# Optimization experiments

Measured on AMD Instinct MI355X. Metric: run time of the kernel, lower is better.

The kernel has to match this reference:

```python
import jax, jax.numpy as jnp
import numpy as np

N = 8192   # nodes
E = 32768  # edges
D = 512    # out_features (node/edge feature dim); in_features = 2*D
DEG = 16   # max neighbors / incident edges per node
DEP = 8    # max node deps per edge
K = 3      # hops (opt.Node_K)


def _padded_idx(k1, k2, rows, width, hi, min_deg):
    # random index lists padded with -1 at the tail
    idx = jax.random.randint(k1, (rows, width), 0, hi, dtype=jnp.int32)
    deg = jax.random.randint(k2, (rows,), min_deg, width + 1, dtype=jnp.int32)
    return jnp.where(jnp.arange(width, dtype=jnp.int32)[None, :] < deg[:, None], idx, -1)


def setup_inputs():
    key = jax.random.key(0)
    ks = jax.random.split(key, 16)
    f32 = jnp.float32
    fw_input = jax.random.normal(ks[0], (N, D), f32)
    bw_input = jax.random.normal(ks[1], (N, D), f32)
    edge_embs = jax.random.normal(ks[2], (E, D), f32)
    fw_adj = _padded_idx(ks[3], ks[4], N, DEG, N, 1)
    bw_adj = _padded_idx(ks[5], ks[6], N, DEG, N, 1)
    fw_edgeid = _padded_idx(ks[7], ks[8], N, DEG, E, 0)
    bw_edgeid = _padded_idx(ks[9], ks[10], N, DEG, E, 0)
    fw_edgedep = _padded_idx(ks[11], ks[12], E, DEP, N, 1)
    bw_edgedep = _padded_idx(ks[13], ks[14], E, DEP, N, 1)
    kp = jax.random.split(ks[15], 3)
    s2 = np.float32(1.0 / np.sqrt(2 * D))
    s3 = np.float32(1.0 / np.sqrt(3 * D))
    Wfc = jax.random.normal(kp[0], (2 * D, D), f32) * s2
    bfc = jnp.zeros((D,), f32)
    Wbc = jax.random.normal(kp[1], (2 * D, D), f32) * s2
    bbc = jnp.zeros((D,), f32)
    Wedge = jax.random.normal(kp[2], (3 * D, D), f32) * s3
    bedge = jnp.zeros((D,), f32)
    return dict(fw_input=fw_input, bw_input=bw_input, edge_embs=edge_embs,
                fw_adj=fw_adj, bw_adj=bw_adj, fw_edgeid=fw_edgeid, bw_edgeid=bw_edgeid,
                fw_edgedep=fw_edgedep, bw_edgedep=bw_edgedep,
                Wfc=Wfc, bfc=bfc, Wbc=Wbc, bbc=bbc, Wedge=Wedge, bedge=bedge)


def _masked_sum(x, idx):
    # gather rows of x at idx (-1 = padding), return masked sum and count
    m = (idx >= 0)
    g = x[jnp.maximum(idx, 0)] * m[..., None].astype(x.dtype)  # [rows, width, D]
    return g.sum(axis=1), m.sum(axis=1)


def _nbr_mean(nodes, adj, edge_embs, eids):
    # mean over (edge embeddings of incident edges ++ neighbor node features)
    s1, c1 = _masked_sum(nodes, adj)
    s2, c2 = _masked_sum(edge_embs, eids)
    cnt = (c1 + c2).astype(nodes.dtype)
    return (s1 + s2) / cnt[:, None]


def _forward(fw_input, bw_input, edge_embs, fw_adj, bw_adj, fw_edgeid, bw_edgeid,
             fw_edgedep, bw_edgedep, Wfc, bfc, Wbc, bbc, Wedge, bedge):
    for k in range(K):
        fmean = _nbr_mean(fw_input, fw_adj, edge_embs, fw_edgeid)
        bmean = _nbr_mean(bw_input, bw_adj, edge_embs, bw_edgeid)
        fh = jnp.concatenate([fw_input, fmean], axis=-1) @ Wfc + bfc
        bh = jnp.concatenate([bw_input, bmean], axis=-1) @ Wbc + bbc
        if k < K - 1:
            fh = jax.nn.relu(fh)
            bh = jax.nn.relu(bh)
        fw_input, bw_input = fh, bh
        if k < K - 1:  # edge update (uses the freshly updated node features)
            fs, fcnt = _masked_sum(fw_input, fw_edgedep)
            bs, bcnt = _masked_sum(bw_input, bw_edgedep)
            fdep = fs / fcnt.astype(fs.dtype)[:, None]
            bdep = bs / bcnt.astype(bs.dtype)[:, None]
            edge_embs = jax.nn.relu(
                jnp.concatenate([edge_embs, fdep, bdep], axis=-1) @ Wedge + bedge)
    return fw_input, bw_input


def reference(fw_input, bw_input, edge_embs, fw_adj, bw_adj, fw_edgeid, bw_edgeid,
              fw_edgedep, bw_edgedep, Wfc, bfc, Wbc, bbc, Wedge, bedge):
    return _forward(fw_input, bw_input, edge_embs, fw_adj, bw_adj, fw_edgeid, bw_edgeid,
                    fw_edgedep, bw_edgedep, Wfc, bfc, Wbc, bbc, Wedge, bedge)
```

## Files before the change

### kernel.cpp

```cpp
#include <hip/hip_runtime.h>
#include <hip/hip_bf16.h>

#define N_NODES 8192
#define N_EDGES 32768
#define DFEAT   512

typedef __attribute__((ext_vector_type(8))) short          bf16x8;
typedef __attribute__((ext_vector_type(4))) float          f32x4;
typedef __attribute__((ext_vector_type(8))) unsigned short u16x8;

__device__ __forceinline__ float bf2f(unsigned short u) {
  union { unsigned int i; float f; } x; x.i = ((unsigned int)u) << 16; return x.f;
}
__device__ __forceinline__ unsigned short f2bf(float f) {
  __hip_bfloat16 h = __float2bfloat16(f);
  return *reinterpret_cast<unsigned short*>(&h);
}

#define GLDS16(gp, lp) __builtin_amdgcn_global_load_lds( \
    (const __attribute__((address_space(1))) void*)(gp),  \
    (__attribute__((address_space(3))) void*)(lp), 16, 0, 0)

#define KEEP16(a) asm volatile("" :: \
  "v"(a[0]), "v"(a[1]), "v"(a[2]),  "v"(a[3]),  "v"(a[4]),  "v"(a[5]),  "v"(a[6]),  "v"(a[7]), \
  "v"(a[8]), "v"(a[9]), "v"(a[10]), "v"(a[11]), "v"(a[12]), "v"(a[13]), "v"(a[14]), "v"(a[15]))

__global__ void transpose_w3(const float* __restrict__ W0, const float* __restrict__ W1,
                             const float* __restrict__ W2,
                             unsigned short* __restrict__ T0, unsigned short* __restrict__ T1,
                             unsigned short* __restrict__ T2) {
  __shared__ float tile[32][33];
  const float* W; unsigned short* WT; int K;
  if (blockIdx.z == 0)      { W = W0; WT = T0; K = 1024; }
  else if (blockIdx.z == 1) { W = W1; WT = T1; K = 1024; }
  else                      { W = W2; WT = T2; K = 1536; }
  const int k0 = blockIdx.x * 32, n0 = blockIdx.y * 32;
  if (k0 >= K) return;
  const int tx = threadIdx.x, ty = threadIdx.y;
  #pragma unroll
  for (int i = ty; i < 32; i += 8)
    tile[i][tx] = W[(long)(k0 + i) * DFEAT + n0 + tx];
  __syncthreads();
  #pragma unroll
  for (int i = ty; i < 32; i += 8)
    WT[(long)(n0 + i) * K + k0 + tx] = f2bf(tile[tx][i]);
}

__global__ void cvt3(const float* __restrict__ a, const float* __restrict__ b,
                     const float* __restrict__ c,
                     unsigned short* __restrict__ da, unsigned short* __restrict__ db,
                     unsigned short* __restrict__ dc, long na, long nc) {
  long i = ((long)blockIdx.x * blockDim.x + threadIdx.x) * 4;
  const float* s; unsigned short* d; long off;
  if (i < na)           { s = a; d = da; off = i; }
  else if (i < 2 * na)  { s = b; d = db; off = i - na; }
  else if (i < 2 * na + nc) { s = c; d = dc; off = i - 2 * na; }
  else return;
  float4 v = *reinterpret_cast<const float4*>(&s[off]);
  ushort4 o = { f2bf(v.x), f2bf(v.y), f2bf(v.z), f2bf(v.w) };
  *reinterpret_cast<ushort4*>(&d[off]) = o;
}

__global__ __launch_bounds__(256, 2) void nbr_mean2(
    const unsigned short* __restrict__ nodesF, const unsigned short* __restrict__ nodesB,
    const unsigned short* __restrict__ edges,
    const int* __restrict__ adjF, const int* __restrict__ adjB,
    const int* __restrict__ eidF, const int* __restrict__ eidB,
    unsigned short* __restrict__ dstF, unsigned short* __restrict__ dstB) {
  const int wave = threadIdx.x >> 6, lane = threadIdx.x & 63;
  const int n = blockIdx.x * 4 + wave;
  const unsigned short* nodes; const int* adj; const int* eid; unsigned short* dst;
  if (blockIdx.y == 0) { nodes = nodesF; adj = adjF; eid = eidF; dst = dstF; }
  else                 { nodes = nodesB; adj = adjB; eid = eidB; dst = dstB; }
  const int c0 = lane * 8;

  int ia[16], ie[16];
  {
    const int4* pa = reinterpret_cast<const int4*>(adj + (long)n * 16);
    const int4* pe = reinterpret_cast<const int4*>(eid + (long)n * 16);
    #pragma unroll
    for (int q = 0; q < 4; ++q) {
      int4 t = pa[q];
      ia[q * 4] = t.x; ia[q * 4 + 1] = t.y; ia[q * 4 + 2] = t.z; ia[q * 4 + 3] = t.w;
      int4 u = pe[q];
      ie[q * 4] = u.x; ie[q * 4 + 1] = u.y; ie[q * 4 + 2] = u.z; ie[q * 4 + 3] = u.w;
    }
  }

  u16x8 va[16], ve[16];
  #pragma unroll
  for (int j = 0; j < 16; ++j) {
    const int a = ia[j] >= 0 ? ia[j] : 0;
    va[j] = *reinterpret_cast<const u16x8*>(&nodes[(long)a * DFEAT + c0]);
  }
  #pragma unroll
  for (int j = 0; j < 16; ++j) {
    const int a = ie[j] >= 0 ? ie[j] : 0;
    ve[j] = *reinterpret_cast<const u16x8*>(&edges[(long)a * DFEAT + c0]);
  }
  KEEP16(va);
  KEEP16(ve);

  float s[8] = {0, 0, 0, 0, 0, 0, 0, 0};
  int cnt = 0;
  #pragma unroll
  for (int j = 0; j < 16; ++j) {
    if (ia[j] >= 0) {
      ++cnt;
      #pragma unroll
      for (int i = 0; i < 8; ++i) s[i] += bf2f(va[j][i]);
    }
  }
  #pragma unroll
  for (int j = 0; j < 16; ++j) {
    if (ie[j] >= 0) {
      ++cnt;
      #pragma unroll
      for (int i = 0; i < 8; ++i) s[i] += bf2f(ve[j][i]);
    }
  }
  const float inv = 1.0f / (float)cnt;
  u16x8 o;
  #pragma unroll
  for (int i = 0; i < 8; ++i) o[i] = f2bf(s[i] * inv);
  *reinterpret_cast<u16x8*>(&dst[(long)n * DFEAT + c0]) = o;
}

__global__ __launch_bounds__(256, 2) void edge_fuse(
    const unsigned short* __restrict__ Pf, const unsigned short* __restrict__ Pb,
    const unsigned short* __restrict__ Ge,
    const int* __restrict__ fdep, const int* __restrict__ bdep,
    unsigned short* __restrict__ Een) {
  const int wave = threadIdx.x >> 6, lane = threadIdx.x & 63;
  const int e = blockIdx.x * 4 + wave;
  const int c0 = lane * 8;

  int idx[16];
  {
    const int4* pf = reinterpret_cast<const int4*>(fdep + (long)e * 8);
    const int4* pb = reinterpret_cast<const int4*>(bdep + (long)e * 8);
    #pragma unroll
    for (int q = 0; q < 2; ++q) {
      int4 t = pf[q];
      idx[q * 4] = t.x; idx[q * 4 + 1] = t.y; idx[q * 4 + 2] = t.z; idx[q * 4 + 3] = t.w;
      int4 u = pb[q];
      idx[8 + q * 4] = u.x; idx[8 + q * 4 + 1] = u.y; idx[8 + q * 4 + 2] = u.z; idx[8 + q * 4 + 3] = u.w;
    }
  }

  const u16x8 gv = *reinterpret_cast<const u16x8*>(&Ge[(long)e * DFEAT + c0]);

  u16x8 v[16];
  #pragma unroll
  for (int j = 0; j < 8; ++j) {
    const int a = idx[j] >= 0 ? idx[j] : 0;
    v[j] = *reinterpret_cast<const u16x8*>(&Pf[(long)a * DFEAT + c0]);
  }
  #pragma unroll
  for (int j = 0; j < 8; ++j) {
    const int a = idx[8 + j] >= 0 ? idx[8 + j] : 0;
    v[8 + j] = *reinterpret_cast<const u16x8*>(&Pb[(long)a * DFEAT + c0]);
  }
  KEEP16(v);

  float sf[8] = {0, 0, 0, 0, 0, 0, 0, 0};
  float sb[8] = {0, 0, 0, 0, 0, 0, 0, 0};
  int fc = 0, bc = 0;
  #pragma unroll
  for (int j = 0; j < 8; ++j) {
    if (idx[j] >= 0) {
      ++fc;
      #pragma unroll
      for (int i = 0; i < 8; ++i) sf[i] += bf2f(v[j][i]);
    }
  }
  #pragma unroll
  for (int j = 0; j < 8; ++j) {
    if (idx[8 + j] >= 0) {
      ++bc;
      #pragma unroll
      for (int i = 0; i < 8; ++i) sb[i] += bf2f(v[8 + j][i]);
    }
  }
  const float invf = 1.0f / (float)fc, invb = 1.0f / (float)bc;
  u16x8 o;
  #pragma unroll
  for (int i = 0; i < 8; ++i) {
    float x = bf2f(gv[i]) + sf[i] * invf + sb[i] * invb;
    o[i] = f2bf(fmaxf(x, 0.0f));
  }
  *reinterpret_cast<u16x8*>(&Een[(long)e * DFEAT + c0]) = o;
}

struct GArg {
  const unsigned short* A0;
  const unsigned short* A1;
  const unsigned short* Bt;
  const float* bias;
  unsigned short* outb;
  float* outf;
};

template<int K, int LDB, int NSEG, int SWZQ, bool RELU, bool BIAS, bool BF16OUT>
__global__ __launch_bounds__(256, 2) void gemm2(GArg ga, GArg gb) {
  const GArg g = blockIdx.z ? gb : ga;
  __shared__ unsigned short As[128][32];
  __shared__ unsigned short Bs[128][32];
  const int tid = threadIdx.x;
  const int wave = tid >> 6, lane = tid & 63;
  const int bid = blockIdx.x;
  const int swz = (bid & 7) * SWZQ + (bid >> 3);
  const long brow = (long)(swz >> 2) * 128;
  const int bcol = (swz & 3) * 128;
  const int wr = (wave >> 1) * 64, wc = (wave & 1) * 64;

  f32x4 acc[4][4] = {};

  const int srow = lane >> 2;
  const int scol = (lane & 3) * 8;
  const int rb = wave * 32;
  unsigned short* As0 = &As[rb][0];
  unsigned short* As1 = &As[rb + 16][0];
  unsigned short* Bs0 = &Bs[rb][0];
  unsigned short* Bs1 = &Bs[rb + 16][0];

  const int fr = lane & 15;
  const int fk = (lane >> 4) * 8;

  for (int kt = 0; kt < K / 32; ++kt) {
    const unsigned short* Aseg;
    int kcol;
    if (NSEG == 1) { Aseg = g.A0; kcol = kt * 32; }
    else           { Aseg = (kt < 16) ? g.A0 : g.A1; kcol = (kt & 15) * 32; }
    GLDS16(Aseg + (brow + rb + srow) * DFEAT + kcol + scol, As0);
    GLDS16(Aseg + (brow + rb + 16 + srow) * DFEAT + kcol + scol, As1);
    const long bk = (long)kt * 32;
    GLDS16(g.Bt + (long)(bcol + rb + srow) * LDB + bk + scol, Bs0);
    GLDS16(g.Bt + (long)(bcol + rb + 16 + srow) * LDB + bk + scol, Bs1);
    __syncthreads();
    bf16x8 af[4], bfr[4];
    #pragma unroll
    for (int m = 0; m < 4; ++m) af[m] = *reinterpret_cast<const bf16x8*>(&As[wr + m * 16 + fr][fk]);
    #pragma unroll
    for (int n = 0; n < 4; ++n) bfr[n] = *reinterpret_cast<const bf16x8*>(&Bs[wc + n * 16 + fr][fk]);
    #pragma unroll
    for (int m = 0; m < 4; ++m)
      #pragma unroll
      for (int n = 0; n < 4; ++n)
        acc[m][n] = __builtin_amdgcn_mfma_f32_16x16x32_bf16(af[m], bfr[n], acc[m][n], 0, 0, 0);
    __syncthreads();
  }

  #pragma unroll
  for (int n = 0; n < 4; ++n) {
    const int col = bcol + wc + n * 16 + fr;
    float bv = 0.0f;
    if (BIAS) bv = g.bias[col];
    #pragma unroll
    for (int m = 0; m < 4; ++m) {
      const long row0 = brow + wr + m * 16 + (lane >> 4) * 4;
      #pragma unroll
      for (int i = 0; i < 4; ++i) {
        float v = acc[m][n][i] + bv;
        if (RELU) v = fmaxf(v, 0.0f);
        if (BF16OUT) g.outb[(row0 + i) * DFEAT + col] = f2bf(v);
        else         g.outf[(row0 + i) * DFEAT + col] = v;
      }
    }
  }
}

extern "C" void kernel_launch(void* const* d_in, const int* in_sizes, int n_in,
                              void* d_out, int out_size, void* d_ws, size_t ws_size,
                              hipStream_t stream) {
  const float* fw_in   = (const float*)d_in[0];
  const float* bw_in   = (const float*)d_in[1];
  const float* edge_in = (const float*)d_in[2];
  const int* fw_adj    = (const int*)d_in[3];
  const int* bw_adj    = (const int*)d_in[4];
  const int* fw_eid    = (const int*)d_in[5];
  const int* bw_eid    = (const int*)d_in[6];
  const int* fw_dep    = (const int*)d_in[7];
  const int* bw_dep    = (const int*)d_in[8];
  const float* Wfc     = (const float*)d_in[9];
  const float* bfc     = (const float*)d_in[10];
  const float* Wbc     = (const float*)d_in[11];
  const float* bbc     = (const float*)d_in[12];
  const float* Wedge   = (const float*)d_in[13];
  const float* bedge   = (const float*)d_in[14];
  float* out_f = (float*)d_out;

  char* w = (char*)d_ws;
  auto alloc = [&](size_t b) { char* p = w; w += (b + 255) & ~(size_t)255; return p; };
  const size_t nodeB = (size_t)N_NODES * DFEAT * 2;
  const size_t edgeB = (size_t)N_EDGES * DFEAT * 2;
  unsigned short* Ff0 = (unsigned short*)alloc(nodeB);
  unsigned short* Ff1 = (unsigned short*)alloc(nodeB);
  unsigned short* Fb0 = (unsigned short*)alloc(nodeB);
  unsigned short* Fb1 = (unsigned short*)alloc(nodeB);
  unsigned short* Mf  = (unsigned short*)alloc(nodeB);
  unsigned short* Mb  = (unsigned short*)alloc(nodeB);
  unsigned short* Pf  = (unsigned short*)alloc(nodeB);
  unsigned short* Pb  = (unsigned short*)alloc(nodeB);
  unsigned short* Ee0 = (unsigned short*)alloc(edgeB);
  unsigned short* Ee1 = (unsigned short*)alloc(edgeB);
  unsigned short* Ge  = (unsigned short*)alloc(edgeB);
  unsigned short* WfT = (unsigned short*)alloc((size_t)1024 * 512 * 2);
  unsigned short* WbT = (unsigned short*)alloc((size_t)1024 * 512 * 2);
  unsigned short* WeT = (unsigned short*)alloc((size_t)1536 * 512 * 2);
  if ((size_t)(w - (char*)d_ws) > ws_size) return;

  transpose_w3<<<dim3(48, 16, 3), dim3(32, 8), 0, stream>>>(Wfc, Wbc, Wedge, WfT, WbT, WeT);
  {
    const long nn = (long)N_NODES * DFEAT, ne = (long)N_EDGES * DFEAT;
    const long tot = 2 * nn + ne;
    cvt3<<<(int)(tot / 4 / 256), 256, 0, stream>>>(fw_in, bw_in, edge_in, Ff0, Fb0, Ee0, nn, ne);
  }

  unsigned short *Ffc = Ff0, *Ffn = Ff1, *Fbc = Fb0, *Fbn = Fb1, *Eec = Ee0, *Een = Ee1;

  for (int k = 0; k < 3; ++k) {
    nbr_mean2<<<dim3(N_NODES / 4, 2), 256, 0, stream>>>(
        Ffc, Fbc, Eec, fw_adj, bw_adj, fw_eid, bw_eid, Mf, Mb);
    if (k < 2) {
      gemm2<1024, 1024, 2, 32, true, true, true><<<dim3(256, 1, 2), 256, 0, stream>>>(
          GArg{Ffc, Mf, WfT, bfc, Ffn, nullptr}, GArg{Fbc, Mb, WbT, bbc, Fbn, nullptr});
      gemm2<512, 1536, 1, 32, false, false, true><<<dim3(256, 1, 2), 256, 0, stream>>>(
          GArg{Ffn, nullptr, WeT + 512, nullptr, Pf, nullptr},
          GArg{Fbn, nullptr, WeT + 1024, nullptr, Pb, nullptr});
      gemm2<512, 1536, 1, 128, false, true, true><<<dim3(1024, 1, 1), 256, 0, stream>>>(
          GArg{Eec, nullptr, WeT, bedge, Ge, nullptr},
          GArg{Eec, nullptr, WeT, bedge, Ge, nullptr});
      edge_fuse<<<N_EDGES / 4, 256, 0, stream>>>(Pf, Pb, Ge, fw_dep, bw_dep, Een);
      unsigned short* t;
      t = Ffc; Ffc = Ffn; Ffn = t;
      t = Fbc; Fbc = Fbn; Fbn = t;
      t = Eec; Eec = Een; Een = t;
    } else {
      gemm2<1024, 1024, 2, 32, false, true, false><<<dim3(256, 1, 2), 256, 0, stream>>>(
          GArg{Ffc, Mf, WfT, bfc, nullptr, out_f},
          GArg{Fbc, Mb, WbT, bbc, nullptr, out_f + (long)N_NODES * DFEAT});
    }
  }
}
```

Measured before the change: 533.1 us.

## Merge edge-projection GEMMs into one launch and stage gather waits with inline loads

Replaces the two edge-update GEMM launches (node projections Pf/Pb and the edge projection Ge) with a single gemm3 kernel. It dispatches 1536 blocks across the three problems using a swizzled block id, which removes one launch and balances the tail. The gather kernels now issue loads through inline asm global_load_dwordx4 and explicit vmcnt waits. This lets nbr_mean start summing neighbor rows while edge rows are still in flight. Hand-written waitcnt is fragile: it relies on the compiler not inserting other vector-memory ops between the loads and the waits.

```diff
diff --git a/kernel.cpp b/kernel.cpp
--- a/kernel.cpp
+++ b/kernel.cpp
@@ -21,9 +21,13 @@
     (const __attribute__((address_space(1))) void*)(gp),  \
     (__attribute__((address_space(3))) void*)(lp), 16, 0, 0)
 
-#define KEEP16(a) asm volatile("" :: \
-  "v"(a[0]), "v"(a[1]), "v"(a[2]),  "v"(a[3]),  "v"(a[4]),  "v"(a[5]),  "v"(a[6]),  "v"(a[7]), \
-  "v"(a[8]), "v"(a[9]), "v"(a[10]), "v"(a[11]), "v"(a[12]), "v"(a[13]), "v"(a[14]), "v"(a[15]))
+__device__ __forceinline__ void gload16(u16x8& d, const unsigned short* p) {
+  asm volatile("global_load_dwordx4 %0, %1, off" : "=v"(d) : "v"(p));
+}
+#define WAIT_VM(N) do { \
+  asm volatile("s_waitcnt vmcnt(" #N ")" ::: "memory"); \
+  __builtin_amdgcn_sched_barrier(0); \
+} while (0)
 
 __global__ void transpose_w3(const float* __restrict__ W0, const float* __restrict__ W1,
                              const float* __restrict__ W2,
@@ -91,18 +95,17 @@
   #pragma unroll
   for (int j = 0; j < 16; ++j) {
     const int a = ia[j] >= 0 ? ia[j] : 0;
-    va[j] = *reinterpret_cast<const u16x8*>(&nodes[(long)a * DFEAT + c0]);
+    gload16(va[j], &nodes[(long)a * DFEAT + c0]);
   }
   #pragma unroll
   for (int j = 0; j < 16; ++j) {
     const int a = ie[j] >= 0 ? ie[j] : 0;
-    ve[j] = *reinterpret_cast<const u16x8*>(&edges[(long)a * DFEAT + c0]);
-  }
-  KEEP16(va);
-  KEEP16(ve);
+    gload16(ve[j], &edges[(long)a * DFEAT + c0]);
+  }
 
   float s[8] = {0, 0, 0, 0, 0, 0, 0, 0};
   int cnt = 0;
+  WAIT_VM(16);
   #pragma unroll
   for (int j = 0; j < 16; ++j) {
     if (ia[j] >= 0) {
@@ -111,6 +114,7 @@
       for (int i = 0; i < 8; ++i) s[i] += bf2f(va[j][i]);
     }
   }
+  WAIT_VM(0);
   #pragma unroll
   for (int j = 0; j < 16; ++j) {
     if (ie[j] >= 0) {
@@ -148,20 +152,19 @@
     }
   }
 
-  const u16x8 gv = *reinterpret_cast<const u16x8*>(&Ge[(long)e * DFEAT + c0]);
-
-  u16x8 v[16];
+  u16x8 gv, v[16];
+  gload16(gv, &Ge[(long)e * DFEAT + c0]);
   #pragma unroll
   for (int j = 0; j < 8; ++j) {
     const int a = idx[j] >= 0 ? idx[j] : 0;
-    v[j] = *reinterpret_cast<const u16x8*>(&Pf[(long)a * DFEAT + c0]);
+    gload16(v[j], &Pf[(long)a * DFEAT + c0]);
   }
   #pragma unroll
   for (int j = 0; j < 8; ++j) {
     const int a = idx[8 + j] >= 0 ? idx[8 + j] : 0;
-    v[8 + j] = *reinterpret_cast<const u16x8*>(&Pb[(long)a * DFEAT + c0]);
-  }
-  KEEP16(v);
+    gload16(v[8 + j], &Pb[(long)a * DFEAT + c0]);
+  }
+  WAIT_VM(0);
 
   float sf[8] = {0, 0, 0, 0, 0, 0, 0, 0};
   float sb[8] = {0, 0, 0, 0, 0, 0, 0, 0};
@@ -266,6 +269,68 @@
         if (BF16OUT) g.outb[(row0 + i) * DFEAT + col] = f2bf(v);
         else         g.outf[(row0 + i) * DFEAT + col] = v;
       }
+    }
+  }
+}
+
+__global__ __launch_bounds__(256, 2) void gemm3(GArg ga, GArg gb, GArg gc) {
+  __shared__ unsigned short As[128][32];
+  __shared__ unsigned short Bs[128][32];
+  const int tid = threadIdx.x;
+  const int wave = tid >> 6, lane = tid & 63;
+  const int bid = blockIdx.x;
+  const int swz = (bid & 7) * 192 + (bid >> 3);
+  GArg g; int base;
+  if (swz < 256)      { g = ga; base = swz; }
+  else if (swz < 512) { g = gb; base = swz - 256; }
+  else                { g = gc; base = swz - 512; }
+  const long brow = (long)(base >> 2) * 128;
+  const int bcol = (base & 3) * 128;
+  const int wr = (wave >> 1) * 64, wc = (wave & 1) * 64;
+
+  f32x4 acc[4][4] = {};
+
+  const int srow = lane >> 2;
+  const int scol = (lane & 3) * 8;
+  const int rb = wave * 32;
+  unsigned short* As0 = &As[rb][0];
+  unsigned short* As1 = &As[rb + 16][0];
+  unsigned short* Bs0 = &Bs[rb][0];
+  unsigned short* Bs1 = &Bs[rb + 16][0];
+
+  const int fr = lane & 15;
+  const int fk = (lane >> 4) * 8;
+
+  for (int kt = 0; kt < 16; ++kt) {
+    const int kcol = kt * 32;
+    GLDS16(g.A0 + (brow + rb + srow) * DFEAT + kcol + scol, As0);
+    GLDS16(g.A0 + (brow + rb + 16 + srow) * DFEAT + kcol + scol, As1);
+    GLDS16(g.Bt + (long)(bcol + rb + srow) * 1536 + kcol + scol, Bs0);
+    GLDS16(g.Bt + (long)(bcol + rb + 16 + srow) * 1536 + kcol + scol, Bs1);
+    __syncthreads();
+    bf16x8 af[4], bfr[4];
+    #pragma unroll
+    for (int m = 0; m < 4; ++m) af[m] = *reinterpret_cast<const bf16x8*>(&As[wr + m * 16 + fr][fk]);
+    #pragma unroll
+    for (int n = 0; n < 4; ++n) bfr[n] = *reinterpret_cast<const bf16x8*>(&Bs[wc + n * 16 + fr][fk]);
+    #pragma unroll
+    for (int m = 0; m < 4; ++m)
+      #pragma unroll
+      for (int n = 0; n < 4; ++n)
+        acc[m][n] = __builtin_amdgcn_mfma_f32_16x16x32_bf16(af[m], bfr[n], acc[m][n], 0, 0, 0);
+    __syncthreads();
+  }
+
+  #pragma unroll
+  for (int n = 0; n < 4; ++n) {
+    const int col = bcol + wc + n * 16 + fr;
+    const float bv = g.bias ? g.bias[col] : 0.0f;
+    #pragma unroll
+    for (int m = 0; m < 4; ++m) {
+      const long row0 = brow + wr + m * 16 + (lane >> 4) * 4;
+      #pragma unroll
+      for (int i = 0; i < 4; ++i)
+        g.outb[(row0 + i) * DFEAT + col] = f2bf(acc[m][n][i] + bv);
     }
   }
 }
@@ -325,11 +390,9 @@
     if (k < 2) {
       gemm2<1024, 1024, 2, 32, true, true, true><<<dim3(256, 1, 2), 256, 0, stream>>>(
           GArg{Ffc, Mf, WfT, bfc, Ffn, nullptr}, GArg{Fbc, Mb, WbT, bbc, Fbn, nullptr});
-      gemm2<512, 1536, 1, 32, false, false, true><<<dim3(256, 1, 2), 256, 0, stream>>>(
+      gemm3<<<dim3(1536), 256, 0, stream>>>(
           GArg{Ffn, nullptr, WeT + 512, nullptr, Pf, nullptr},
-          GArg{Fbn, nullptr, WeT + 1024, nullptr, Pb, nullptr});
-      gemm2<512, 1536, 1, 128, false, true, true><<<dim3(1024, 1, 1), 256, 0, stream>>>(
-          GArg{Eec, nullptr, WeT, bedge, Ge, nullptr},
+          GArg{Fbn, nullptr, WeT + 1024, nullptr, Pb, nullptr},
           GArg{Eec, nullptr, WeT, bedge, Ge, nullptr});
       edge_fuse<<<N_EDGES / 4, 256, 0, stream>>>(Pf, Pb, Ge, fw_dep, bw_dep, Een);
       unsigned short* t;
```

New measurement: 526.4 us. No clear change (-1.3%).

## Fuse edge GEMM into neighbor-mean kernel, widen GEMM K-tile with swizzled LDS

Applied to the files above, without the earlier changes.

Every fifth block of the neighbor-mean launch now runs one tile of the edge-embedding GEMM, so the gather and the GEMM share one launch and can overlap. This drops a separate kernel launch per hop. The GEMM core moves from a 32-wide to a 64-wide K tile, with an XOR-swizzled LDS layout that halves the number of sync rounds and is meant to reduce bank conflicts. The gather kernels issue their loads through inline asm with explicit vmcnt waits, so the first batch of gathered rows can be summed while the rest are still in flight. The trade-offs are a larger LDS footprint, mixed block types in one launch with a relaxed occupancy bound, and hand-managed wait counts.

```diff
diff --git a/kernel.cpp b/kernel.cpp
--- a/kernel.cpp
+++ b/kernel.cpp
@@ -21,9 +21,13 @@
     (const __attribute__((address_space(1))) void*)(gp),  \
     (__attribute__((address_space(3))) void*)(lp), 16, 0, 0)
 
-#define KEEP16(a) asm volatile("" :: \
-  "v"(a[0]), "v"(a[1]), "v"(a[2]),  "v"(a[3]),  "v"(a[4]),  "v"(a[5]),  "v"(a[6]),  "v"(a[7]), \
-  "v"(a[8]), "v"(a[9]), "v"(a[10]), "v"(a[11]), "v"(a[12]), "v"(a[13]), "v"(a[14]), "v"(a[15]))
+__device__ __forceinline__ void gload16(u16x8& d, const unsigned short* p) {
+  asm volatile("global_load_dwordx4 %0, %1, off" : "=v"(d) : "v"(p));
+}
+#define WAIT_VM(N) do { \
+  asm volatile("s_waitcnt vmcnt(" #N ")" ::: "memory"); \
+  __builtin_amdgcn_sched_barrier(0); \
+} while (0)
 
 __global__ void transpose_w3(const float* __restrict__ W0, const float* __restrict__ W1,
                              const float* __restrict__ W2,
@@ -61,17 +65,120 @@
   *reinterpret_cast<ushort4*>(&d[off]) = o;
 }
 
-__global__ __launch_bounds__(256, 2) void nbr_mean2(
+struct GArg {
+  const unsigned short* A0;
+  const unsigned short* A1;
+  const unsigned short* Bt;
+  const float* bias;
+  unsigned short* outb;
+  float* outf;
+};
+
+template<int K, int LDB, int NSEG, bool RELU, bool BIAS, bool BF16OUT>
+__device__ __forceinline__ void gemm_core(GArg g, long brow, int bcol,
+                                          unsigned short (*As)[64],
+                                          unsigned short (*Bs)[64]) {
+  const int tid = threadIdx.x;
+  const int wave = tid >> 6, lane = tid & 63;
+  const int wr = (wave >> 1) * 64, wc = (wave & 1) * 64;
+  f32x4 acc[4][4] = {};
+
+  const int rb = wave * 32;
+  const int sl8 = lane >> 3;
+  const int scol = ((lane & 7) ^ sl8) * 8;
+  const int fr = lane & 15;
+  const int fk = (lane >> 4) * 8;
+
+  for (int kt = 0; kt < K / 64; ++kt) {
+    const unsigned short* Aseg; int kcol;
+    if (NSEG == 1) { Aseg = g.A0; kcol = kt * 64; }
+    else           { Aseg = (kt < 8) ? g.A0 : g.A1; kcol = (kt & 7) * 64; }
+    #pragma unroll
+    for (int c = 0; c < 4; ++c)
+      GLDS16(Aseg + (brow + rb + 8 * c + sl8) * DFEAT + kcol + scol, &As[rb + 8 * c][0]);
+    const long bk = (long)kt * 64;
+    #pragma unroll
+    for (int c = 0; c < 4; ++c)
+      GLDS16(g.Bt + (long)(bcol + rb + 8 * c + sl8) * LDB + bk + scol, &Bs[rb + 8 * c][0]);
+    __syncthreads();
+    #pragma unroll
+    for (int kk = 0; kk < 2; ++kk) {
+      bf16x8 af[4], bfr[4];
+      #pragma unroll
+      for (int m = 0; m < 4; ++m) {
+        const int R = wr + m * 16 + fr;
+        af[m] = *reinterpret_cast<const bf16x8*>(&As[R][(kk * 32 + fk) ^ ((R & 7) * 8)]);
+      }
+      #pragma unroll
+      for (int n = 0; n < 4; ++n) {
+        const int R = wc + n * 16 + fr;
+        bfr[n] = *reinterpret_cast<const bf16x8*>(&Bs[R][(kk * 32 + fk) ^ ((R & 7) * 8)]);
+      }
+      #pragma unroll
+      for (int m = 0; m < 4; ++m)
+        #pragma unroll
+        for (int n = 0; n < 4; ++n)
+          acc[m][n] = __builtin_amdgcn_mfma_f32_16x16x32_bf16(af[m], bfr[n], acc[m][n], 0, 0, 0);
+    }
+    __syncthreads();
+  }
+
+  #pragma unroll
+  for (int n = 0; n < 4; ++n) {
+    const int col = bcol + wc + n * 16 + fr;
+    float bv = 0.0f;
+    if (BIAS) bv = g.bias[col];
+    #pragma unroll
+    for (int m = 0; m < 4; ++m) {
+      const long row0 = brow + wr + m * 16 + (lane >> 4) * 4;
+      #pragma unroll
+      for (int i = 0; i < 4; ++i) {
+        float v = acc[m][n][i] + bv;
+        if (RELU) v = fmaxf(v, 0.0f);
+        if (BF16OUT) g.outb[(row0 + i) * DFEAT + col] = f2bf(v);
+        else         g.outf[(row0 + i) * DFEAT + col] = v;
+      }
+    }
+  }
+}
+
+template<int K, int LDB, int NSEG, int SWZQ, bool RELU, bool BIAS, bool BF16OUT>
+__global__ __launch_bounds__(256, 2) void gemmK(GArg ga, GArg gb) {
+  __shared__ unsigned short As[128][64];
+  __shared__ unsigned short Bs[128][64];
+  const GArg g = blockIdx.z ? gb : ga;
+  const int bid = blockIdx.x;
+  const int swz = (bid & 7) * SWZQ + (bid >> 3);
+  gemm_core<K, LDB, NSEG, RELU, BIAS, BF16OUT>(
+      g, (long)(swz >> 2) * 128, (swz & 3) * 128, As, Bs);
+}
+
+__global__ __launch_bounds__(256) void fused_nbr_ge(
     const unsigned short* __restrict__ nodesF, const unsigned short* __restrict__ nodesB,
     const unsigned short* __restrict__ edges,
     const int* __restrict__ adjF, const int* __restrict__ adjB,
     const int* __restrict__ eidF, const int* __restrict__ eidB,
-    unsigned short* __restrict__ dstF, unsigned short* __restrict__ dstB) {
+    unsigned short* __restrict__ dstF, unsigned short* __restrict__ dstB,
+    GArg ge, int hasGe) {
+  __shared__ unsigned short As[128][64];
+  __shared__ unsigned short Bs[128][64];
+  int bid = blockIdx.x;
+  if (hasGe) {
+    if ((bid % 5) == 4) {
+      const int gid = bid / 5;
+      const int swz = (gid & 7) * 128 + (gid >> 3);
+      gemm_core<512, 1536, 1, false, true, true>(
+          ge, (long)(swz >> 2) * 128, (swz & 3) * 128, As, Bs);
+      return;
+    }
+    bid = (bid / 5) * 4 + (bid % 5);
+  }
   const int wave = threadIdx.x >> 6, lane = threadIdx.x & 63;
-  const int n = blockIdx.x * 4 + wave;
+  const int side = bid >> 11;
+  const int n = (bid & 2047) * 4 + wave;
   const unsigned short* nodes; const int* adj; const int* eid; unsigned short* dst;
-  if (blockIdx.y == 0) { nodes = nodesF; adj = adjF; eid = eidF; dst = dstF; }
-  else                 { nodes = nodesB; adj = adjB; eid = eidB; dst = dstB; }
+  if (side == 0) { nodes = nodesF; adj = adjF; eid = eidF; dst = dstF; }
+  else           { nodes = nodesB; adj = adjB; eid = eidB; dst = dstB; }
   const int c0 = lane * 8;
 
   int ia[16], ie[16];
@@ -91,18 +198,17 @@
   #pragma unroll
   for (int j = 0; j < 16; ++j) {
     const int a = ia[j] >= 0 ? ia[j] : 0;
-    va[j] = *reinterpret_cast<const u16x8*>(&nodes[(long)a * DFEAT + c0]);
+    gload16(va[j], &nodes[(long)a * DFEAT + c0]);
   }
   #pragma unroll
   for (int j = 0; j < 16; ++j) {
     const int a = ie[j] >= 0 ? ie[j] : 0;
-    ve[j] = *reinterpret_cast<const u16x8*>(&edges[(long)a * DFEAT + c0]);
-  }
-  KEEP16(va);
-  KEEP16(ve);
+    gload16(ve[j], &edges[(long)a * DFEAT + c0]);
+  }
 
   float s[8] = {0, 0, 0, 0, 0, 0, 0, 0};
   int cnt = 0;
+  WAIT_VM(16);
   #pragma unroll
   for (int j = 0; j < 16; ++j) {
     if (ia[j] >= 0) {
@@ -111,6 +217,7 @@
       for (int i = 0; i < 8; ++i) s[i] += bf2f(va[j][i]);
     }
   }
+  WAIT_VM(0);
   #pragma unroll
   for (int j = 0; j < 16; ++j) {
     if (ie[j] >= 0) {
@@ -148,20 +255,19 @@
     }
   }
 
-  const u16x8 gv = *reinterpret_cast<const u16x8*>(&Ge[(long)e * DFEAT + c0]);
-
-  u16x8 v[16];
+  u16x8 gv, v[16];
+  gload16(gv, &Ge[(long)e * DFEAT + c0]);
   #pragma unroll
   for (int j = 0; j < 8; ++j) {
     const int a = idx[j] >= 0 ? idx[j] : 0;
-    v[j] = *reinterpret_cast<const u16x8*>(&Pf[(long)a * DFEAT + c0]);
+    gload16(v[j], &Pf[(long)a * DFEAT + c0]);
   }
   #pragma unroll
   for (int j = 0; j < 8; ++j) {
     const int a = idx[8 + j] >= 0 ? idx[8 + j] : 0;
-    v[8 + j] = *reinterpret_cast<const u16x8*>(&Pb[(long)a * DFEAT + c0]);
-  }
-  KEEP16(v);
+    gload16(v[8 + j], &Pb[(long)a * DFEAT + c0]);
+  }
+  WAIT_VM(0);
 
   float sf[8] = {0, 0, 0, 0, 0, 0, 0, 0};
   float sb[8] = {0, 0, 0, 0, 0, 0, 0, 0};
@@ -190,84 +296,6 @@
     o[i] = f2bf(fmaxf(x, 0.0f));
   }
   *reinterpret_cast<u16x8*>(&Een[(long)e * DFEAT + c0]) = o;
-}
-
-struct GArg {
-  const unsigned short* A0;
-  const unsigned short* A1;
-  const unsigned short* Bt;
-  const float* bias;
-  unsigned short* outb;
-  float* outf;
-};
-
-template<int K, int LDB, int NSEG, int SWZQ, bool RELU, bool BIAS, bool BF16OUT>
-__global__ __launch_bounds__(256, 2) void gemm2(GArg ga, GArg gb) {
-  const GArg g = blockIdx.z ? gb : ga;
-  __shared__ unsigned short As[128][32];
-  __shared__ unsigned short Bs[128][32];
-  const int tid = threadIdx.x;
-  const int wave = tid >> 6, lane = tid & 63;
-  const int bid = blockIdx.x;
-  const int swz = (bid & 7) * SWZQ + (bid >> 3);
-  const long brow = (long)(swz >> 2) * 128;
-  const int bcol = (swz & 3) * 128;
-  const int wr = (wave >> 1) * 64, wc = (wave & 1) * 64;
-
-  f32x4 acc[4][4] = {};
-
-  const int srow = lane >> 2;
-  const int scol = (lane & 3) * 8;
-  const int rb = wave * 32;
-  unsigned short* As0 = &As[rb][0];
-  unsigned short* As1 = &As[rb + 16][0];
-  unsigned short* Bs0 = &Bs[rb][0];
-  unsigned short* Bs1 = &Bs[rb + 16][0];
-
-  const int fr = lane & 15;
-  const int fk = (lane >> 4) * 8;
-
-  for (int kt = 0; kt < K / 32; ++kt) {
-    const unsigned short* Aseg;
-    int kcol;
-    if (NSEG == 1) { Aseg = g.A0; kcol = kt * 32; }
-    else           { Aseg = (kt < 16) ? g.A0 : g.A1; kcol = (kt & 15) * 32; }
-    GLDS16(Aseg + (brow + rb + srow) * DFEAT + kcol + scol, As0);
-    GLDS16(Aseg + (brow + rb + 16 + srow) * DFEAT + kcol + scol, As1);
-    const long bk = (long)kt * 32;
-    GLDS16(g.Bt + (long)(bcol + rb + srow) * LDB + bk + scol, Bs0);
-    GLDS16(g.Bt + (long)(bcol + rb + 16 + srow) * LDB + bk + scol, Bs1);
-    __syncthreads();
-    bf16x8 af[4], bfr[4];
-    #pragma unroll
-    for (int m = 0; m < 4; ++m) af[m] = *reinterpret_cast<const bf16x8*>(&As[wr + m * 16 + fr][fk]);
-    #pragma unroll
-    for (int n = 0; n < 4; ++n) bfr[n] = *reinterpret_cast<const bf16x8*>(&Bs[wc + n * 16 + fr][fk]);
-    #pragma unroll
-    for (int m = 0; m < 4; ++m)
-      #pragma unroll
-      for (int n = 0; n < 4; ++n)
-        acc[m][n] = __builtin_amdgcn_mfma_f32_16x16x32_bf16(af[m], bfr[n], acc[m][n], 0, 0, 0);
-    __syncthreads();
-  }
-
-  #pragma unroll
-  for (int n = 0; n < 4; ++n) {
-    const int col = bcol + wc + n * 16 + fr;
-    float bv = 0.0f;
-    if (BIAS) bv = g.bias[col];
-    #pragma unroll
-    for (int m = 0; m < 4; ++m) {
-      const long row0 = brow + wr + m * 16 + (lane >> 4) * 4;
-      #pragma unroll
-      for (int i = 0; i < 4; ++i) {
-        float v = acc[m][n][i] + bv;
-        if (RELU) v = fmaxf(v, 0.0f);
-        if (BF16OUT) g.outb[(row0 + i) * DFEAT + col] = f2bf(v);
-        else         g.outf[(row0 + i) * DFEAT + col] = v;
-      }
-    }
-  }
 }
 
 extern "C" void kernel_launch(void* const* d_in, const int* in_sizes, int n_in,
@@ -320,24 +348,23 @@
   unsigned short *Ffc = Ff0, *Ffn = Ff1, *Fbc = Fb0, *Fbn = Fb1, *Eec = Ee0, *Een = Ee1;
 
   for (int k = 0; k < 3; ++k) {
-    nbr_mean2<<<dim3(N_NODES / 4, 2), 256, 0, stream>>>(
-        Ffc, Fbc, Eec, fw_adj, bw_adj, fw_eid, bw_eid, Mf, Mb);
+    const int hasGe = (k < 2) ? 1 : 0;
+    fused_nbr_ge<<<hasGe ? 5120 : 4096, 256, 0, stream>>>(
+        Ffc, Fbc, Eec, fw_adj, bw_adj, fw_eid, bw_eid, Mf, Mb,
+        GArg{Eec, nullptr, WeT, bedge, Ge, nullptr}, hasGe);
     if (k < 2) {
-      gemm2<1024, 1024, 2, 32, true, true, true><<<dim3(256, 1, 2), 256, 0, stream>>>(
+      gemmK<1024, 1024, 2, 32, true, true, true><<<dim3(256, 1, 2), 256, 0, stream>>>(
           GArg{Ffc, Mf, WfT, bfc, Ffn, nullptr}, GArg{Fbc, Mb, WbT, bbc, Fbn, nullptr});
-      gemm2<512, 1536, 1, 32, false, false, true><<<dim3(256, 1, 2), 256, 0, stream>>>(
+      gemmK<512, 1536, 1, 32, false, false, true><<<dim3(256, 1, 2), 256, 0, stream>>>(
           GArg{Ffn, nullptr, WeT + 512, nullptr, Pf, nullptr},
           GArg{Fbn, nullptr, WeT + 1024, nullptr, Pb, nullptr});
-      gemm2<512, 1536, 1, 128, false, true, true><<<dim3(1024, 1, 1), 256, 0, stream>>>(
-          GArg{Eec, nullptr, WeT, bedge, Ge, nullptr},
-          GArg{Eec, nullptr, WeT, bedge, Ge, nullptr});
       edge_fuse<<<N_EDGES / 4, 256, 0, stream>>>(Pf, Pb, Ge, fw_dep, bw_dep, Een);
       unsigned short* t;
       t = Ffc; Ffc = Ffn; Ffn = t;
       t = Fbc; Fbc = Fbn; Fbn = t;
       t = Eec; Eec = Een; Een = t;
     } else {
-      gemm2<1024, 1024, 2, 32, false, true, false><<<dim3(256, 1, 2), 256, 0, stream>>>(
+      gemmK<1024, 1024, 2, 32, false, true, false><<<dim3(256, 1, 2), 256, 0, stream>>>(
           GArg{Ffc, Mf, WfT, bfc, nullptr, out_f},
           GArg{Fbc, Mb, WbT, bbc, nullptr, out_f + (long)N_NODES * DFEAT});
     }
```

Result: faster. 500.8 us (-6.1%).
